# Performance work log

Measured on AMD Instinct MI355X. Metric: run time of the kernel, lower is better.

The kernel has to match this reference:

```python
import jax, jax.numpy as jnp
import numpy as np

D_MODEL = 1024
NUM_HEADS = 16
ALPHA = 1.0


def setup_inputs() -> dict:
    key = jax.random.key(0)
    ks = jax.random.split(key, 6)
    bs, L, d = 2, 2048, D_MODEL
    s = 1.0 / np.sqrt(d)
    mu = jax.random.normal(ks[0], (bs, L, d), dtype=jnp.float32)
    sigma = jax.random.uniform(ks[1], (bs, L, d), dtype=jnp.float32)
    W_qkv_mu = (jax.random.normal(ks[2], (d, 3 * d), dtype=jnp.float32) * s)
    b_qkv_mu = jnp.zeros((3 * d,), dtype=jnp.float32)
    W_qkv_sigma = (jax.random.normal(ks[3], (d, 3 * d), dtype=jnp.float32) * s)
    b_qkv_sigma = jnp.zeros((3 * d,), dtype=jnp.float32)
    W_out = (jax.random.normal(ks[4], (d, d), dtype=jnp.float32) * s)
    b_out = jnp.zeros((d,), dtype=jnp.float32)
    return {"mu": mu, "sigma": sigma,
            "W_qkv_mu": W_qkv_mu, "b_qkv_mu": b_qkv_mu,
            "W_qkv_sigma": W_qkv_sigma, "b_qkv_sigma": b_qkv_sigma,
            "W_out": W_out, "b_out": b_out}


def reference(mu, sigma, W_qkv_mu, b_qkv_mu, W_qkv_sigma, b_qkv_sigma, W_out, b_out):
    bs, L, d = mu.shape
    H = NUM_HEADS
    dk = d // H

    def heads(x):  # [b, L, d] -> [b, H, L, dk]
        return x.reshape(bs, L, H, dk).transpose(0, 2, 1, 3)

    Qm, Km, Vm = (heads(t) for t in jnp.split(mu @ W_qkv_mu + b_qkv_mu, 3, axis=-1))
    Qs, Ks, Vs = (heads(t) for t in jnp.split(sigma @ W_qkv_sigma + b_qkv_sigma, 3, axis=-1))

    # Wasserstein^2 = sum((Qm-Km)^2) + sum((Qs-Ks)^2), expanded so the
    # pairwise [b,H,L,L,dk] broadcast tensor is never materialized.
    sq_q = jnp.sum(Qm * Qm, -1) + jnp.sum(Qs * Qs, -1)  # [b,H,L]
    sq_k = jnp.sum(Km * Km, -1) + jnp.sum(Ks * Ks, -1)  # [b,H,L]
    cross = (jnp.einsum('bhid,bhjd->bhij', Qm, Km)
             + jnp.einsum('bhid,bhjd->bhij', Qs, Ks))   # [b,H,L,L]
    W2 = sq_q[..., :, None] + sq_k[..., None, :] - 2.0 * cross
    W = jnp.sqrt(jnp.maximum(W2, 0.0))

    similarity = jnp.exp(-ALPHA * W)
    attn = jax.nn.softmax(similarity, axis=-1)  # softmax OVER the similarities (as in torch code)

    def merge(x):  # [b,H,L,dk] -> [b,L,d]
        return x.transpose(0, 2, 1, 3).reshape(bs, L, d)

    out_mu = merge(jnp.einsum('bhij,bhjd->bhid', attn, Vm)) @ W_out + b_out
    out_sigma = merge(jnp.einsum('bhij,bhjd->bhid', attn, Vs)) @ W_out + b_out
    return out_mu, out_sigma
```

## Files before the change

kernel.cpp:

```cpp
#include <hip/hip_runtime.h>
#include <hip/hip_bf16.h>

#define LSEQ   2048
#define DK     64
#define NH     16
#define BS     2
#define DMODEL 1024
#define BH     (BS*NH)
#define MTOT   (BS*LSEQ)

typedef __attribute__((ext_vector_type(8))) short bf16x8;
typedef __attribute__((ext_vector_type(4))) float f32x4;
typedef __attribute__((ext_vector_type(16))) float f32x16;

#define MFMA16(a,b,c) __builtin_amdgcn_mfma_f32_16x16x32_bf16((a),(b),(c),0,0,0)
#define MFMA32(a,b,c) __builtin_amdgcn_mfma_f32_32x32x16_bf16((a),(b),(c),0,0,0)
#define GLD_LDS(g,l) __builtin_amdgcn_global_load_lds((const __attribute__((address_space(1))) void*)(g), (__attribute__((address_space(3))) void*)(l), 16, 0, 0)

#define L2E   1.4426950408889634f
#define L2E2  2.0813689810056077f

__device__ __forceinline__ short f2bs(float f) {
  union { __hip_bfloat16 h; short s; } u; u.h = __float2bfloat16(f); return u.s;
}
__device__ __forceinline__ float b2f(unsigned short s) {
  union { unsigned u; float f; } v; v.u = ((unsigned)s) << 16; return v.f;
}
__device__ __forceinline__ unsigned short f2bs_c(float f) {
  union { float f; unsigned u; } v; v.f = f;
  return (unsigned short)((v.u + 0x8000u) >> 16);
}
__device__ __forceinline__ unsigned pk2c(float lo, float hi) {
  union { float f; unsigned u; } a, b; a.f = lo; b.f = hi;
  return ((a.u + 0x8000u) >> 16) | ((b.u + 0x8000u) & 0xffff0000u);
}
__device__ __forceinline__ unsigned pk2(float lo, float hi) {
  return (unsigned)(unsigned short)f2bs(lo) | (((unsigned)(unsigned short)f2bs(hi)) << 16);
}
__device__ __forceinline__ float fexp2(float x) {
  float r; asm("v_exp_f32 %0, %1" : "=v"(r) : "v"(x)); return r;
}
__device__ __forceinline__ float fexp2n(float x) {
  float r; asm("v_exp_f32 %0, -%1" : "=v"(r) : "v"(x)); return r;
}
__device__ __forceinline__ unsigned cvtpk(float lo, float hi) {
  unsigned r; asm("v_cvt_pk_bf16_f32 %0, %1, %2" : "=v"(r) : "v"(lo), "v"(hi)); return r;
}

__global__ __launch_bounds__(256) void cvt2_k(const float* __restrict__ a,
                                              const float* __restrict__ b,
                                              short* __restrict__ oa,
                                              short* __restrict__ ob, int n8) {
  int total = n8 * 2;
  for (int i = blockIdx.x * blockDim.x + threadIdx.x; i < total; i += gridDim.x * blockDim.x) {
    int sel = i >= n8;
    int j = sel ? i - n8 : i;
    const float4* p = (const float4*)(sel ? b : a) + (size_t)j * 2;
    float4 x = p[0], y = p[1];
    uint4 o;
    o.x = pk2(x.x, x.y); o.y = pk2(x.z, x.w);
    o.z = pk2(y.x, y.y); o.w = pk2(y.z, y.w);
    ((uint4*)(sel ? ob : oa))[j] = o;
  }
}

__global__ __launch_bounds__(256) void cvt_tr_all_k(
    const float* __restrict__ Wqm, const float* __restrict__ Wqs, const float* __restrict__ Wo,
    short* __restrict__ Wqm_t, short* __restrict__ Wqs_t, short* __restrict__ Wo_t) {
  __shared__ float tile[32][33];
  int id = blockIdx.x;
  const float* W; short* Wt; int Ncols, bx;
  if (id < 3072)      { W = Wqm; Wt = Wqm_t; Ncols = 3072; bx = id % 96; id /= 96; }
  else if (id < 6144) { id -= 3072; W = Wqs; Wt = Wqs_t; Ncols = 3072; bx = id % 96; id /= 96; }
  else                { id -= 6144; W = Wo;  Wt = Wo_t;  Ncols = 1024; bx = id % 32; id /= 32; }
  int n0 = bx * 32, k0 = id * 32;
  int t = threadIdx.x;
#pragma unroll
  for (int i = 0; i < 4; ++i) {
    int idx = t + i * 256; int r = idx >> 5, c = idx & 31;
    tile[r][c] = W[(size_t)(k0 + r) * Ncols + n0 + c];
  }
  __syncthreads();
#pragma unroll
  for (int i = 0; i < 4; ++i) {
    int idx = t + i * 256; int r = idx >> 5, c = idx & 31;
    Wt[(size_t)(n0 + r) * 1024 + k0 + c] = f2bs(tile[c][r]);
  }
}

__global__ __launch_bounds__(256) void qkv_gemm_k(
    const short* __restrict__ Amu, const short* __restrict__ Asg,
    const short* __restrict__ Wqm_t, const short* __restrict__ Wqs_t,
    const float* __restrict__ bqm, const float* __restrict__ bqs,
    short* __restrict__ Qm, short* __restrict__ Km, short* __restrict__ VmT,
    short* __restrict__ Qs, short* __restrict__ Ks, short* __restrict__ VsT) {
  __shared__ short As[128 * 64];
  __shared__ short Bs[128 * 64];
  int ny = blockIdx.y;
  int sg = ny >= 24;
  int n0 = (sg ? ny - 24 : ny) * 128;
  const short* A  = sg ? Asg : Amu;
  const short* Bt = sg ? Wqs_t : Wqm_t;
  const float* bias = sg ? bqs : bqm;
  short* Qb  = sg ? Qs : Qm;
  short* Kb  = sg ? Ks : Km;
  short* VTb = sg ? VsT : VmT;

  int tid = threadIdx.x, w = tid >> 6, ln = tid & 63, lg = ln >> 4, lr = ln & 15;
  int m0 = blockIdx.x * 128;
  int wr = w >> 1, wc = w & 1;
  f32x4 acc[4][4] = {};

  for (int k0 = 0; k0 < 1024; k0 += 64) {
    __syncthreads();
#pragma unroll
    for (int i = 0; i < 4; ++i) {
      int cb = w * 64 + i * 256;
      int c = cb + ln;
      GLD_LDS(A  + (size_t)(m0 + (c >> 3)) * 1024 + k0 + (c & 7) * 8, &As[cb * 8]);
      GLD_LDS(Bt + (size_t)(n0 + (c >> 3)) * 1024 + k0 + (c & 7) * 8, &Bs[cb * 8]);
    }
    __syncthreads();
#pragma unroll
    for (int kh = 0; kh < 2; ++kh) {
      bf16x8 af[4], bfr[4];
#pragma unroll
      for (int mi = 0; mi < 4; ++mi)
        af[mi] = *(const bf16x8*)&As[(wr * 64 + mi * 16 + lr) * 64 + kh * 32 + lg * 8];
#pragma unroll
      for (int ni = 0; ni < 4; ++ni)
        bfr[ni] = *(const bf16x8*)&Bs[(wc * 64 + ni * 16 + lr) * 64 + kh * 32 + lg * 8];
#pragma unroll
      for (int mi = 0; mi < 4; ++mi)
#pragma unroll
        for (int ni = 0; ni < 4; ++ni)
          acc[mi][ni] = MFMA16(af[mi], bfr[ni], acc[mi][ni]);
    }
  }

#pragma unroll
  for (int ni = 0; ni < 4; ++ni) {
    int n = n0 + wc * 64 + ni * 16 + lr;
    float bv = bias[n];
    int part = n >> 10, cc = n & 1023, hh = cc >> 6, dd = cc & 63;
#pragma unroll
    for (int mi = 0; mi < 4; ++mi) {
      int mbase = m0 + wr * 64 + mi * 16 + 4 * lg;
      float vv[4];
#pragma unroll
      for (int r = 0; r < 4; ++r) vv[r] = acc[mi][ni][r] + bv;
      if (part == 2) {
        int b = mbase >> 11, tok = mbase & 2047, bh = b * NH + hh;
        uint2 pk; pk.x = pk2c(vv[0], vv[1]); pk.y = pk2c(vv[2], vv[3]);
        *(uint2*)&VTb[((size_t)bh * DK + dd) * LSEQ + tok] = pk;
      } else {
        short* dst = (part == 0) ? Qb : Kb;
#pragma unroll
        for (int r = 0; r < 4; ++r) {
          int m = mbase + r;
          int b = m >> 11, tok = m & 2047, bh = b * NH + hh;
          dst[((size_t)bh * LSEQ + tok) * DK + dd] = (short)f2bs_c(vv[r]);
        }
      }
    }
  }
}

__global__ __launch_bounds__(256) void gemm128_k(
    const short* __restrict__ A, const short* __restrict__ Bt,
    const float* __restrict__ bias, float* __restrict__ outF) {
  __shared__ short As[128 * 64];
  __shared__ short Bs[128 * 64];
  int tid = threadIdx.x, w = tid >> 6, ln = tid & 63, lg = ln >> 4, lr = ln & 15;
  int m0 = blockIdx.x * 128, n0 = blockIdx.y * 128;
  int wr = w >> 1, wc = w & 1;
  f32x4 acc[4][4] = {};

  for (int k0 = 0; k0 < 1024; k0 += 64) {
    __syncthreads();
#pragma unroll
    for (int i = 0; i < 4; ++i) {
      int cb = w * 64 + i * 256;
      int c = cb + ln;
      GLD_LDS(A  + (size_t)(m0 + (c >> 3)) * 1024 + k0 + (c & 7) * 8, &As[cb * 8]);
      GLD_LDS(Bt + (size_t)(n0 + (c >> 3)) * 1024 + k0 + (c & 7) * 8, &Bs[cb * 8]);
    }
    __syncthreads();
#pragma unroll
    for (int kh = 0; kh < 2; ++kh) {
      bf16x8 af[4], bfr[4];
#pragma unroll
      for (int mi = 0; mi < 4; ++mi)
        af[mi] = *(const bf16x8*)&As[(wr * 64 + mi * 16 + lr) * 64 + kh * 32 + lg * 8];
#pragma unroll
      for (int ni = 0; ni < 4; ++ni)
        bfr[ni] = *(const bf16x8*)&Bs[(wc * 64 + ni * 16 + lr) * 64 + kh * 32 + lg * 8];
#pragma unroll
      for (int mi = 0; mi < 4; ++mi)
#pragma unroll
        for (int ni = 0; ni < 4; ++ni)
          acc[mi][ni] = MFMA16(af[mi], bfr[ni], acc[mi][ni]);
    }
  }

#pragma unroll
  for (int ni = 0; ni < 4; ++ni) {
    int n = n0 + wc * 64 + ni * 16 + lr;
    float bv = bias[n];
#pragma unroll
    for (int mi = 0; mi < 4; ++mi) {
      int mbase = m0 + wr * 64 + mi * 16 + 4 * lg;
#pragma unroll
      for (int r = 0; r < 4; ++r)
        outF[(size_t)(mbase + r) * 1024 + n] = acc[mi][ni][r] + bv;
    }
  }
}

__global__ __launch_bounds__(256) void norms_k(
    const short* __restrict__ Qm, const short* __restrict__ Qs,
    const short* __restrict__ Km, const short* __restrict__ Ks,
    float* __restrict__ sqq, float* __restrict__ sqk) {
  int id = blockIdx.x * 256 + threadIdx.x;
  int row = id & 65535;
  const short* p1 = (id < 65536) ? Qm : Km;
  const short* p2 = (id < 65536) ? Qs : Ks;
  float* outp = (id < 65536) ? sqq : sqk;
  const uint4* a = (const uint4*)(p1 + (size_t)row * DK);
  const uint4* b = (const uint4*)(p2 + (size_t)row * DK);
  float s = 0.f;
#pragma unroll
  for (int i = 0; i < 8; ++i) {
    uint4 x = a[i], y = b[i];
    unsigned vx[4] = {x.x, x.y, x.z, x.w};
    unsigned vy[4] = {y.x, y.y, y.z, y.w};
#pragma unroll
    for (int j = 0; j < 4; ++j) {
      float l1 = b2f((unsigned short)(vx[j] & 0xffff)), h1 = b2f((unsigned short)(vx[j] >> 16));
      float l2 = b2f((unsigned short)(vy[j] & 0xffff)), h2 = b2f((unsigned short)(vy[j] >> 16));
      s += l1 * l1 + h1 * h1 + l2 * l2 + h2 * h2;
    }
  }
  outp[row] = s * L2E2;
}

__global__ __launch_bounds__(512, 2) void attn_k(
    const short* __restrict__ Qm, const short* __restrict__ Km, const short* __restrict__ VmT,
    const short* __restrict__ Qs, const short* __restrict__ Ks, const short* __restrict__ VsT,
    const float* __restrict__ sqq, const float* __restrict__ sqk,
    short* __restrict__ Om, short* __restrict__ Os) {
  int id = blockIdx.y * 8 + blockIdx.x;
  int pid = id >> 3;
  int bh = (id & 7) * 4 + (pid >> 3);
  int q0 = (pid & 7) * 256;
  int tid = threadIdx.x, w = tid >> 6, ln = tid & 63;
  int l31 = ln & 31, h = ln >> 5;

  __shared__ __align__(16) char pool[65536];
  short* poolS = (short*)pool;

  const size_t bhQ = (size_t)bh * LSEQ * DK;

  int q = q0 + w * 32 + l31;
  bf16x8 qmf[4], qsf[4];
#pragma unroll
  for (int d = 0; d < 4; ++d) {
    qmf[d] = *(const bf16x8*)(Qm + bhQ + (size_t)q * DK + d * 16 + h * 8);
    qsf[d] = *(const bf16x8*)(Qs + bhQ + (size_t)q * DK + d * 16 + h * 8);
  }
  float sqQ = sqq[(size_t)bh * LSEQ + q];
  const float* sqkp = sqk + (size_t)bh * LSEQ;

  const short* sb0;
  {
    int t2 = tid & 255;
    int rr = t2 >> 3;
    int cs = ((t2 & 7) ^ (rr & 7) ^ ((rr >> 3) & 3)) * 8;
    sb0 = ((tid < 256) ? Km : Ks) + bhQ + (size_t)rr * DK + cs;
  }
  const short* sb1;
  {
    int row = tid >> 3;
    int c = (tid & 7) ^ (row & 7);
    sb1 = ((c < 4) ? (VmT + ((size_t)bh * DK + row) * LSEQ + c * 8)
                   : (VsT + ((size_t)bh * DK + row) * LSEQ + (c - 4) * 8));
  }

  f32x16 acc[4] = {};
  float prs = 0.f;

  const int krow = l31;
  const int kswz = ((krow & 7) ^ ((krow >> 3) & 3)) << 4;
  const int NT = LSEQ / 32;

#define ISSUE_TILE(tt, bb) do {                                          \
    GLD_LDS(sb0 + (size_t)(tt) * 2048, poolS + (bb) * 8192 + w * 512);   \
    GLD_LDS(sb1 + (size_t)(tt) * 32,   poolS + (bb) * 8192 + 4096 + w * 512); \
  } while (0)

#define QK_TILE(bb, sdst) do {                                           \
    const char* kb_ = (const char*)(poolS + (bb) * 8192);                \
    __builtin_amdgcn_s_setprio(1);                                       \
    _Pragma("unroll")                                                    \
    for (int d = 0; d < 4; ++d) {                                        \
      bf16x8 am = *(const bf16x8*)(kb_ + krow * 128 + ((d * 32 + h * 16) ^ kswz)); \
      sdst = MFMA32(am, qmf[d], sdst);                                   \
      bf16x8 as = *(const bf16x8*)(kb_ + 4096 + krow * 128 + ((d * 32 + h * 16) ^ kswz)); \
      sdst = MFMA32(as, qsf[d], sdst);                                   \
    }                                                                    \
    __builtin_amdgcn_s_setprio(0);                                       \
  } while (0)

  ISSUE_TILE(0, 0);
  ISSUE_TILE(1, 1);
  asm volatile("s_waitcnt vmcnt(2)" ::: "memory");
  asm volatile("s_barrier" ::: "memory");
  ISSUE_TILE(2, 2);

  f32x16 s_prev = {};
  QK_TILE(0, s_prev);
  f32x4 rskreg[4];
#pragma unroll
  for (int rq = 0; rq < 4; ++rq)
    rskreg[rq] = *(const f32x4*)&sqkp[8 * rq + 4 * h];

  for (int t = 1; t < NT; ++t) {
    asm volatile("s_waitcnt vmcnt(6)" ::: "memory");
    asm volatile("s_barrier" ::: "memory");
    {
      int tn = (t + 2 < NT) ? (t + 2) : (NT - 1);
      ISSUE_TILE(tn, (t + 2) & 3);
    }

    f32x16 s_cur = {};
    QK_TILE(t & 3, s_cur);

    float pv[16];
#pragma unroll
    for (int rq = 0; rq < 4; ++rq) {
#pragma unroll
      for (int r = 0; r < 4; ++r) {
        int i = rq * 4 + r;
        float w2 = fmaf(-2.f * L2E2, s_prev[i], sqQ + rskreg[rq][r]);
        float wdp = __builtin_amdgcn_sqrtf(fmaxf(w2, 0.f));
        float sim = fexp2n(wdp);
        float p = fexp2(sim * L2E);
        prs += p;
        pv[i] = p;
      }
    }
    unsigned u0 = cvtpk(pv[0], pv[1]),   u1 = cvtpk(pv[2], pv[3]);
    unsigned u2 = cvtpk(pv[4], pv[5]),   u3 = cvtpk(pv[6], pv[7]);
    unsigned u4 = cvtpk(pv[8], pv[9]),   u5 = cvtpk(pv[10], pv[11]);
    unsigned u6 = cvtpk(pv[12], pv[13]), u7 = cvtpk(pv[14], pv[15]);
    asm volatile("v_permlane32_swap_b32 %0, %1" : "+v"(u0), "+v"(u2));
    asm volatile("v_permlane32_swap_b32 %0, %1" : "+v"(u1), "+v"(u3));
    asm volatile("v_permlane32_swap_b32 %0, %1" : "+v"(u4), "+v"(u6));
    asm volatile("v_permlane32_swap_b32 %0, %1" : "+v"(u5), "+v"(u7));
    union { uint4 u; bf16x8 v; } f0, f1;
    f0.u.x = u0; f0.u.y = u1; f0.u.z = u2; f0.u.w = u3;
    f1.u.x = u4; f1.u.y = u5; f1.u.z = u6; f1.u.w = u7;

#pragma unroll
    for (int rq = 0; rq < 4; ++rq)
      rskreg[rq] = *(const f32x4*)&sqkp[t * 32 + 8 * rq + 4 * h];

    {
      const char* vb = (const char*)(poolS + ((t - 1) & 3) * 8192) + 8192;
      __builtin_amdgcn_s_setprio(1);
#pragma unroll
      for (int vblk = 0; vblk < 4; ++vblk) {
        int row = (vblk & 1) * 32 + l31;
        int cb = (vblk >> 1) * 4;
        int sw = row & 7;
        const char* rb = vb + row * 128;
        bf16x8 v0 = *(const bf16x8*)(rb + (((cb + h) ^ sw) << 4));
        bf16x8 v1 = *(const bf16x8*)(rb + (((cb + 2 + h) ^ sw) << 4));
        acc[vblk] = MFMA32(v0, f0.v, acc[vblk]);
        acc[vblk] = MFMA32(v1, f1.v, acc[vblk]);
      }
      __builtin_amdgcn_s_setprio(0);
    }

    s_prev = s_cur;
  }

  asm volatile("s_waitcnt vmcnt(0)" ::: "memory");

  {
    float pv[16];
#pragma unroll
    for (int rq = 0; rq < 4; ++rq) {
#pragma unroll
      for (int r = 0; r < 4; ++r) {
        int i = rq * 4 + r;
        float w2 = fmaf(-2.f * L2E2, s_prev[i], sqQ + rskreg[rq][r]);
        float wdp = __builtin_amdgcn_sqrtf(fmaxf(w2, 0.f));
        float sim = fexp2n(wdp);
        float p = fexp2(sim * L2E);
        prs += p;
        pv[i] = p;
      }
    }
    unsigned u0 = cvtpk(pv[0], pv[1]),   u1 = cvtpk(pv[2], pv[3]);
    unsigned u2 = cvtpk(pv[4], pv[5]),   u3 = cvtpk(pv[6], pv[7]);
    unsigned u4 = cvtpk(pv[8], pv[9]),   u5 = cvtpk(pv[10], pv[11]);
    unsigned u6 = cvtpk(pv[12], pv[13]), u7 = cvtpk(pv[14], pv[15]);
    asm volatile("v_permlane32_swap_b32 %0, %1" : "+v"(u0), "+v"(u2));
    asm volatile("v_permlane32_swap_b32 %0, %1" : "+v"(u1), "+v"(u3));
    asm volatile("v_permlane32_swap_b32 %0, %1" : "+v"(u4), "+v"(u6));
    asm volatile("v_permlane32_swap_b32 %0, %1" : "+v"(u5), "+v"(u7));
    union { uint4 u; bf16x8 v; } f0, f1;
    f0.u.x = u0; f0.u.y = u1; f0.u.z = u2; f0.u.w = u3;
    f1.u.x = u4; f1.u.y = u5; f1.u.z = u6; f1.u.w = u7;

    const char* vb = (const char*)(poolS + ((NT - 1) & 3) * 8192) + 8192;
#pragma unroll
    for (int vblk = 0; vblk < 4; ++vblk) {
      int row = (vblk & 1) * 32 + l31;
      int cb = (vblk >> 1) * 4;
      int sw = row & 7;
      const char* rb = vb + row * 128;
      bf16x8 v0 = *(const bf16x8*)(rb + (((cb + h) ^ sw) << 4));
      bf16x8 v1 = *(const bf16x8*)(rb + (((cb + 2 + h) ^ sw) << 4));
      acc[vblk] = MFMA32(v0, f0.v, acc[vblk]);
      acc[vblk] = MFMA32(v1, f1.v, acc[vblk]);
    }
  }

  prs += __shfl_xor(prs, 32);
  float inv = 1.f / prs;

  int b = bh >> 4, hh = bh & 15;
  size_t orow = ((size_t)(b * LSEQ + q)) * DMODEL + hh * DK;
#pragma unroll
  for (int vblk = 0; vblk < 4; ++vblk) {
    short* obuf = (vblk < 2) ? Om : Os;
    int vbase = (vblk & 1) * 32 + 4 * h;
#pragma unroll
    for (int rq = 0; rq < 4; ++rq) {
      float o0 = acc[vblk][rq * 4 + 0] * inv;
      float o1 = acc[vblk][rq * 4 + 1] * inv;
      float o2 = acc[vblk][rq * 4 + 2] * inv;
      float o3 = acc[vblk][rq * 4 + 3] * inv;
      uint2 pk; pk.x = pk2c(o0, o1); pk.y = pk2c(o2, o3);
      *(uint2*)(obuf + orow + vbase + 8 * rq) = pk;
    }
  }
#undef ISSUE_TILE
#undef QK_TILE
}

extern "C" void kernel_launch(void* const* d_in, const int* in_sizes, int n_in,
                              void* d_out, int out_size, void* d_ws, size_t ws_size,
                              hipStream_t stream) {
  const float* mu    = (const float*)d_in[0];
  const float* sigma = (const float*)d_in[1];
  const float* Wqm   = (const float*)d_in[2];
  const float* bqm   = (const float*)d_in[3];
  const float* Wqs   = (const float*)d_in[4];
  const float* bqs   = (const float*)d_in[5];
  const float* Wo    = (const float*)d_in[6];
  const float* bo    = (const float*)d_in[7];
  float* out = (float*)d_out;
  char* ws = (char*)d_ws;
  const size_t MB = 1u << 20;

  short* Amu   = (short*)(ws + 0);
  short* Asg   = (short*)(ws + 8 * MB);
  short* Wqm_t = (short*)(ws + 16 * MB);
  short* Wqs_t = (short*)(ws + 22 * MB);
  short* Wo_t  = (short*)(ws + 28 * MB);
  short* Qm    = (short*)(ws + 30 * MB);
  short* Km    = (short*)(ws + 38 * MB);
  short* VmT   = (short*)(ws + 46 * MB);
  short* Qs    = (short*)(ws + 54 * MB);
  short* Ks    = (short*)(ws + 62 * MB);
  short* VsT   = (short*)(ws + 70 * MB);
  float* sqq   = (float*)(ws + 78 * MB);
  float* sqk   = (float*)(ws + 78 * MB + 256 * 1024);
  short* Om = Amu;
  short* Os = Asg;

  cvt2_k<<<2048, 256, 0, stream>>>(mu, sigma, Amu, Asg, MTOT * DMODEL / 8);
  cvt_tr_all_k<<<7168, 256, 0, stream>>>(Wqm, Wqs, Wo, Wqm_t, Wqs_t, Wo_t);

  qkv_gemm_k<<<dim3(32, 48), 256, 0, stream>>>(Amu, Asg, Wqm_t, Wqs_t, bqm, bqs,
                                               Qm, Km, VmT, Qs, Ks, VsT);

  norms_k<<<512, 256, 0, stream>>>(Qm, Qs, Km, Ks, sqq, sqk);

  attn_k<<<dim3(8, 32), 512, 0, stream>>>(Qm, Km, VmT, Qs, Ks, VsT, sqq, sqk, Om, Os);

  gemm128_k<<<dim3(64, 8), 256, 0, stream>>>(Om, Wo_t, bo, out);
}
```

Before: 234.1 us.

## Shrink attention blocks to 4 waves with 3-stage LDS ring for more occupancy

The attention kernel now uses 256-thread blocks covering 128 queries each, with twice as many blocks. Each thread issues four global-to-LDS loads per tile instead of two, to cover K and V. The LDS ring drops from four buffers with two tiles in flight to three rotating buffers with one tile prefetched. This cuts LDS per block to 48KB, so three blocks can share a CU, trading prefetch depth and K/V reuse per block for more resident blocks and finer-grained scheduling.

```diff
diff --git a/kernel.cpp b/kernel.cpp
--- a/kernel.cpp
+++ b/kernel.cpp
@@ -244,19 +244,19 @@
   outp[row] = s * L2E2;
 }
 
-__global__ __launch_bounds__(512, 2) void attn_k(
+__global__ __launch_bounds__(256, 3) void attn_k(
     const short* __restrict__ Qm, const short* __restrict__ Km, const short* __restrict__ VmT,
     const short* __restrict__ Qs, const short* __restrict__ Ks, const short* __restrict__ VsT,
     const float* __restrict__ sqq, const float* __restrict__ sqk,
     short* __restrict__ Om, short* __restrict__ Os) {
   int id = blockIdx.y * 8 + blockIdx.x;
   int pid = id >> 3;
-  int bh = (id & 7) * 4 + (pid >> 3);
-  int q0 = (pid & 7) * 256;
+  int bh = (id & 7) * 4 + (pid >> 4);
+  int q0 = (pid & 15) * 128;
   int tid = threadIdx.x, w = tid >> 6, ln = tid & 63;
   int l31 = ln & 31, h = ln >> 5;
 
-  __shared__ __align__(16) char pool[65536];
+  __shared__ __align__(16) char pool[49152];
   short* poolS = (short*)pool;
 
   const size_t bhQ = (size_t)bh * LSEQ * DK;
@@ -271,20 +271,16 @@
   float sqQ = sqq[(size_t)bh * LSEQ + q];
   const float* sqkp = sqk + (size_t)bh * LSEQ;
 
-  const short* sb0;
-  {
-    int t2 = tid & 255;
-    int rr = t2 >> 3;
-    int cs = ((t2 & 7) ^ (rr & 7) ^ ((rr >> 3) & 3)) * 8;
-    sb0 = ((tid < 256) ? Km : Ks) + bhQ + (size_t)rr * DK + cs;
-  }
-  const short* sb1;
-  {
-    int row = tid >> 3;
-    int c = (tid & 7) ^ (row & 7);
-    sb1 = ((c < 4) ? (VmT + ((size_t)bh * DK + row) * LSEQ + c * 8)
-                   : (VsT + ((size_t)bh * DK + row) * LSEQ + (c - 4) * 8));
-  }
+  int rrK = tid >> 3;
+  int csK = ((tid & 7) ^ (rrK & 7) ^ ((rrK >> 3) & 3)) * 8;
+  const short* sKm = Km + bhQ + (size_t)rrK * DK + csK;
+  const short* sKs = Ks + bhQ + (size_t)rrK * DK + csK;
+  int rv = tid >> 3;
+  int cv = (tid & 7) ^ (rv & 7);
+  const short* sV0 = (cv < 4) ? (VmT + ((size_t)bh * DK + rv) * LSEQ + cv * 8)
+                              : (VsT + ((size_t)bh * DK + rv) * LSEQ + (cv - 4) * 8);
+  const short* sV1 = (cv < 4) ? (VmT + ((size_t)bh * DK + rv + 32) * LSEQ + cv * 8)
+                              : (VsT + ((size_t)bh * DK + rv + 32) * LSEQ + (cv - 4) * 8);
 
   f32x16 acc[4] = {};
   float prs = 0.f;
@@ -293,29 +289,30 @@
   const int kswz = ((krow & 7) ^ ((krow >> 3) & 3)) << 4;
   const int NT = LSEQ / 32;
 
-#define ISSUE_TILE(tt, bb) do {                                          \
-    GLD_LDS(sb0 + (size_t)(tt) * 2048, poolS + (bb) * 8192 + w * 512);   \
-    GLD_LDS(sb1 + (size_t)(tt) * 32,   poolS + (bb) * 8192 + 4096 + w * 512); \
+#define ISSUE_TILE(tt, bb) do {                                              \
+    GLD_LDS(sKm + (size_t)(tt) * 2048, poolS + (bb) * 8192 + w * 512);       \
+    GLD_LDS(sKs + (size_t)(tt) * 2048, poolS + (bb) * 8192 + 2048 + w * 512);\
+    GLD_LDS(sV0 + (size_t)(tt) * 32,   poolS + (bb) * 8192 + 4096 + w * 512);\
+    GLD_LDS(sV1 + (size_t)(tt) * 32,   poolS + (bb) * 8192 + 6144 + w * 512);\
   } while (0)
 
-#define QK_TILE(bb, sdst) do {                                           \
-    const char* kb_ = (const char*)(poolS + (bb) * 8192);                \
-    __builtin_amdgcn_s_setprio(1);                                       \
-    _Pragma("unroll")                                                    \
-    for (int d = 0; d < 4; ++d) {                                        \
+#define QK_TILE(bb, sdst) do {                                               \
+    const char* kb_ = (const char*)(poolS + (bb) * 8192);                    \
+    __builtin_amdgcn_s_setprio(1);                                           \
+    _Pragma("unroll")                                                        \
+    for (int d = 0; d < 4; ++d) {                                            \
       bf16x8 am = *(const bf16x8*)(kb_ + krow * 128 + ((d * 32 + h * 16) ^ kswz)); \
-      sdst = MFMA32(am, qmf[d], sdst);                                   \
+      sdst = MFMA32(am, qmf[d], sdst);                                       \
       bf16x8 as = *(const bf16x8*)(kb_ + 4096 + krow * 128 + ((d * 32 + h * 16) ^ kswz)); \
-      sdst = MFMA32(as, qsf[d], sdst);                                   \
-    }                                                                    \
-    __builtin_amdgcn_s_setprio(0);                                       \
+      sdst = MFMA32(as, qsf[d], sdst);                                       \
+    }                                                                        \
+    __builtin_amdgcn_s_setprio(0);                                           \
   } while (0)
 
   ISSUE_TILE(0, 0);
   ISSUE_TILE(1, 1);
-  asm volatile("s_waitcnt vmcnt(2)" ::: "memory");
+  asm volatile("s_waitcnt vmcnt(4)" ::: "memory");
   asm volatile("s_barrier" ::: "memory");
-  ISSUE_TILE(2, 2);
 
   f32x16 s_prev = {};
   QK_TILE(0, s_prev);
@@ -324,16 +321,14 @@
   for (int rq = 0; rq < 4; ++rq)
     rskreg[rq] = *(const f32x4*)&sqkp[8 * rq + 4 * h];
 
+  int ppv = 0, pqk = 1, pwr = 2;
   for (int t = 1; t < NT; ++t) {
-    asm volatile("s_waitcnt vmcnt(6)" ::: "memory");
+    asm volatile("s_waitcnt vmcnt(4)" ::: "memory");
     asm volatile("s_barrier" ::: "memory");
-    {
-      int tn = (t + 2 < NT) ? (t + 2) : (NT - 1);
-      ISSUE_TILE(tn, (t + 2) & 3);
-    }
+    if (t + 1 < NT) ISSUE_TILE(t + 1, pwr);
 
     f32x16 s_cur = {};
-    QK_TILE(t & 3, s_cur);
+    QK_TILE(pqk, s_cur);
 
     float pv[16];
 #pragma unroll
@@ -366,7 +361,7 @@
       rskreg[rq] = *(const f32x4*)&sqkp[t * 32 + 8 * rq + 4 * h];
 
     {
-      const char* vb = (const char*)(poolS + ((t - 1) & 3) * 8192) + 8192;
+      const char* vb = (const char*)(poolS + ppv * 8192) + 8192;
       __builtin_amdgcn_s_setprio(1);
 #pragma unroll
       for (int vblk = 0; vblk < 4; ++vblk) {
@@ -383,6 +378,7 @@
     }
 
     s_prev = s_cur;
+    int tmp = ppv; ppv = pqk; pqk = pwr; pwr = tmp;
   }
 
   asm volatile("s_waitcnt vmcnt(0)" ::: "memory");
@@ -414,7 +410,7 @@
     f0.u.x = u0; f0.u.y = u1; f0.u.z = u2; f0.u.w = u3;
     f1.u.x = u4; f1.u.y = u5; f1.u.z = u6; f1.u.w = u7;
 
-    const char* vb = (const char*)(poolS + ((NT - 1) & 3) * 8192) + 8192;
+    const char* vb = (const char*)(poolS + ppv * 8192) + 8192;
 #pragma unroll
     for (int vblk = 0; vblk < 4; ++vblk) {
       int row = (vblk & 1) * 32 + l31;
@@ -490,7 +486,7 @@
 
   norms_k<<<512, 256, 0, stream>>>(Qm, Qs, Km, Ks, sqq, sqk);
 
-  attn_k<<<dim3(8, 32), 512, 0, stream>>>(Qm, Km, VmT, Qs, Ks, VsT, sqq, sqk, Om, Os);
+  attn_k<<<dim3(8, 64), 256, 0, stream>>>(Qm, Km, VmT, Qs, Ks, VsT, sqq, sqk, Om, Os);
 
   gemm128_k<<<dim3(64, 8), 256, 0, stream>>>(Om, Wo_t, bo, out);
 }
```

Result: slower. 265.2 us (+13.3%).
